# Kernel optimization log

Measured on AMD Instinct MI355X. Metric: run time of the kernel, lower is better.

The kernel has to match this reference:

```python
import jax, jax.numpy as jnp
import numpy as np

N = 100000      # nodes
E = 1600000     # edges (before self-loops)
IN = 128        # in_channels
H = 4           # heads
C = 32          # hidden_channels (per head)
HC = H * C      # 128, LayerNorm dim
NEG_SLOPE = 0.2
LN_EPS = 1e-5


def setup_inputs() -> dict:
    key = jax.random.key(0)
    ks = jax.random.split(key, 8)
    x = jax.random.normal(ks[0], (N, IN), dtype=jnp.float32)
    edge_index = jax.random.randint(ks[1], (2, E), 0, N, dtype=jnp.int64)
    edge_weight = jax.random.uniform(ks[2], (E,), dtype=jnp.float32)
    # GATConv parameters
    W = jax.random.normal(ks[3], (IN, HC), dtype=jnp.float32) * (1.0 / np.sqrt(IN))
    att_src = jax.random.normal(ks[4], (H, C), dtype=jnp.float32) * (1.0 / np.sqrt(C))
    att_dst = jax.random.normal(ks[5], (H, C), dtype=jnp.float32) * (1.0 / np.sqrt(C))
    bias = jnp.zeros((HC,), dtype=jnp.float32)
    # LayerNorm parameters
    gamma = jnp.ones((HC,), dtype=jnp.float32)
    beta = jnp.zeros((HC,), dtype=jnp.float32)
    return {"x": x, "edge_index": edge_index, "edge_weight": edge_weight,
            "W": W, "att_src": att_src, "att_dst": att_dst, "bias": bias,
            "gamma": gamma, "beta": beta}


def reference(x, edge_index, edge_weight, W, att_src, att_dst, bias, gamma, beta):
    # --- GATConv (heads=4, concat, add_self_loops=True) ---
    loops = jnp.arange(N, dtype=edge_index.dtype)
    ei = jnp.concatenate([edge_index, jnp.stack([loops, loops])], axis=1)  # [2, E+N]
    src, dst = ei[0], ei[1]

    xw = (x @ W).reshape(N, H, C)                       # [N, H, C]
    a_src = jnp.sum(xw * att_src, axis=-1)              # [N, H]
    a_dst = jnp.sum(xw * att_dst, axis=-1)              # [N, H]

    # per-edge attention logits, softmax grouped by destination node
    e = jax.nn.leaky_relu(a_src[src] + a_dst[dst], NEG_SLOPE)   # [E+N, H]
    m = jax.ops.segment_max(e, dst, num_segments=N)             # [N, H]
    ex = jnp.exp(e - m[dst])
    denom = jax.ops.segment_sum(ex, dst, num_segments=N)        # [N, H]
    alpha = ex / (denom[dst] + 1e-16)                           # [E+N, H]

    # weighted scatter-add of source features to destinations
    msg = alpha[:, :, None] * xw[src]                           # [E+N, H, C]
    out = jax.ops.segment_sum(msg, dst, num_segments=N)         # [N, H, C]
    out = out.reshape(N, HC) + bias                             # concat heads + bias

    # --- LayerNorm ---
    mu = jnp.mean(out, axis=-1, keepdims=True)
    var = jnp.var(out, axis=-1, keepdims=True)
    return gamma * (out - mu) / jnp.sqrt(var + LN_EPS) + beta
```

## Files before the change

### kernel.cpp

```cpp
#include <hip/hip_runtime.h>
#include <math.h>

#define NN 100000
#define EE 1600000
#define ETOT (EE + NN)
#define NBUK 512
#define NPB 196
#define CHUNK 3125
#define CAP 6144
#define GB 1563

typedef __attribute__((ext_vector_type(8))) short bf16x8;
typedef __attribute__((ext_vector_type(4))) float f32x4;

__device__ __forceinline__ unsigned short f2bf(float f) {
  unsigned int u = __float_as_uint(f);
  u = u + 0x7fffu + ((u >> 16) & 1u);
  return (unsigned short)(u >> 16);
}

__device__ __forceinline__ float lrelu_exp(float e) {
  e = (e > 0.f) ? e : 0.2f * e;
  return __expf(e);
}

__global__ __launch_bounds__(256) void k_gemm(const float* __restrict__ x,
                                              const float* __restrict__ W,
                                              const float* __restrict__ att_src,
                                              const float* __restrict__ att_dst,
                                              const int* __restrict__ ei,
                                              unsigned short* __restrict__ xwb,
                                              float* __restrict__ asrc,
                                              float* __restrict__ adst,
                                              int* __restrict__ H,
                                              int* __restrict__ Sc) {
  __shared__ __align__(16) unsigned short lds[17408];
  __shared__ float satt[256];
  __shared__ int hh[NBUK];
  int tid = threadIdx.x;

  if (blockIdx.x >= GB) {
    int j = blockIdx.x - GB;
    for (int i = tid; i < NBUK; i += 256) hh[i] = 0;
    __syncthreads();
    int e0 = j * CHUNK;
    for (int e = e0 + tid; e < e0 + CHUNK; e += 256) {
      int d = ei[(size_t)EE + e];
      atomicAdd(&hh[d / NPB], 1);
    }
    __syncthreads();
    for (int i = tid; i < NBUK; i += 256) H[j * NBUK + i] = hh[i];
    int* s = (int*)lds;
    int va = hh[tid], vb = hh[tid + 256];
    s[tid] = va;
    __syncthreads();
    for (int off = 1; off < 256; off <<= 1) {
      int tmp = (tid >= off) ? s[tid - off] : 0;
      __syncthreads();
      s[tid] += tmp;
      __syncthreads();
    }
    int Sa = s[tid], SaT = s[255];
    __syncthreads();
    s[tid] = vb;
    __syncthreads();
    for (int off = 1; off < 256; off <<= 1) {
      int tmp = (tid >= off) ? s[tid - off] : 0;
      __syncthreads();
      s[tid] += tmp;
      __syncthreads();
    }
    Sc[j * 512 + tid] = Sa - va;
    Sc[j * 512 + 256 + tid] = SaT + s[tid] - vb;
    return;
  }

  for (int i = tid; i < 16384; i += 256) {
    int k = i >> 7, n = i & 127;
    lds[n * 136 + k] = f2bf(W[i]);
  }
  if (tid < 128) satt[tid] = att_src[tid];
  else satt[tid] = att_dst[tid - 128];
  __syncthreads();

  int wv = tid >> 6, lane = tid & 63;
  int m = lane & 15, q = lane >> 4;
  int r = blockIdx.x * 64 + wv * 16 + m;
  bool rok = (r < NN);

  bf16x8 af[4];
#pragma unroll
  for (int kt = 0; kt < 4; kt++) {
    float4 v0 = make_float4(0.f, 0.f, 0.f, 0.f), v1 = v0;
    if (rok) {
      v0 = ((const float4*)x)[(size_t)r * 32 + kt * 8 + q * 2];
      v1 = ((const float4*)x)[(size_t)r * 32 + kt * 8 + q * 2 + 1];
    }
    af[kt][0] = (short)f2bf(v0.x); af[kt][1] = (short)f2bf(v0.y);
    af[kt][2] = (short)f2bf(v0.z); af[kt][3] = (short)f2bf(v0.w);
    af[kt][4] = (short)f2bf(v1.x); af[kt][5] = (short)f2bf(v1.y);
    af[kt][6] = (short)f2bf(v1.z); af[kt][7] = (short)f2bf(v1.w);
  }

  f32x4 acc[8];
#pragma unroll
  for (int nt = 0; nt < 8; nt++) acc[nt] = (f32x4){0.f, 0.f, 0.f, 0.f};

#pragma unroll
  for (int nt = 0; nt < 8; nt++) {
#pragma unroll
    for (int kt = 0; kt < 4; kt++) {
      bf16x8 bf = *((const bf16x8*)&lds[(nt * 16 + m) * 136 + kt * 32 + q * 8]);
      acc[nt] = __builtin_amdgcn_mfma_f32_16x16x32_bf16(af[kt], bf, acc[nt], 0, 0, 0);
    }
  }

  __syncthreads();
#pragma unroll
  for (int nt = 0; nt < 8; nt++)
#pragma unroll
    for (int rg = 0; rg < 4; rg++)
      lds[(wv * 16 + q * 4 + rg) * 128 + nt * 16 + m] = f2bf(acc[nt][rg]);
  __syncthreads();

  size_t base = (size_t)blockIdx.x * 16384;
  const size_t lim = (size_t)NN * 256;
  for (int i = tid; i < 1024; i += 256) {
    size_t off = base + (size_t)i * 16;
    if (off < lim) *((uint4*)((char*)xwb + off)) = ((const uint4*)lds)[i];
  }

  int row = tid >> 2, h = tid & 3;
  int node = blockIdx.x * 64 + row;
  if (node < NN) {
    float ss = 0.f, sd = 0.f;
#pragma unroll
    for (int cq = 0; cq < 4; cq++) {
      uint4 u = *((const uint4*)&lds[row * 128 + h * 32 + cq * 8]);
      int cb = h * 32 + cq * 8;
      float f0 = __uint_as_float(u.x << 16), f1 = __uint_as_float(u.x & 0xffff0000u);
      float f2 = __uint_as_float(u.y << 16), f3 = __uint_as_float(u.y & 0xffff0000u);
      float f4 = __uint_as_float(u.z << 16), f5 = __uint_as_float(u.z & 0xffff0000u);
      float f6 = __uint_as_float(u.w << 16), f7 = __uint_as_float(u.w & 0xffff0000u);
      ss += f0 * satt[cb] + f1 * satt[cb + 1] + f2 * satt[cb + 2] + f3 * satt[cb + 3] +
            f4 * satt[cb + 4] + f5 * satt[cb + 5] + f6 * satt[cb + 6] + f7 * satt[cb + 7];
      sd += f0 * satt[128 + cb] + f1 * satt[128 + cb + 1] + f2 * satt[128 + cb + 2] +
            f3 * satt[128 + cb + 3] + f4 * satt[128 + cb + 4] + f5 * satt[128 + cb + 5] +
            f6 * satt[128 + cb + 6] + f7 * satt[128 + cb + 7];
    }
    asrc[(size_t)node * 4 + h] = ss;
    adst[(size_t)node * 4 + h] = sd;
  }
}

__global__ __launch_bounds__(512) void k_s1(const int* __restrict__ H,
                                            int* __restrict__ R, int* __restrict__ T) {
  __shared__ int s[512];
  int b = blockIdx.x, t = threadIdx.x;
  int v = H[t * NBUK + b];
  s[t] = v;
  __syncthreads();
  for (int off = 1; off < 512; off <<= 1) {
    int tmp = (t >= off) ? s[t - off] : 0;
    __syncthreads();
    s[t] += tmp;
    __syncthreads();
  }
  R[b * 512 + t] = s[t] - v;
  if (t == 511) T[b] = s[511];
}

__global__ __launch_bounds__(512) void k_s2(const int* __restrict__ T,
                                            int* __restrict__ Base) {
  __shared__ int s2[512];
  int t = threadIdx.x;
  int v = T[t];
  int ncnt = NN - t * NPB;
  ncnt = (ncnt < 0) ? 0 : ((ncnt > NPB) ? NPB : ncnt);
  int w = v + ncnt;
  s2[t] = w;
  __syncthreads();
  for (int off = 1; off < 512; off <<= 1) {
    int tb = (t >= off) ? s2[t - off] : 0;
    __syncthreads();
    s2[t] += tb;
    __syncthreads();
  }
  Base[t] = s2[t] - w;
}

__global__ __launch_bounds__(256) void k_p3(const int* __restrict__ ei,
                                            const int* __restrict__ Sc,
                                            int* __restrict__ tmpb) {
  __shared__ int cur[NBUK];
  __shared__ int stage2[CHUNK];
  int j = blockIdx.x, t = threadIdx.x;
  for (int b = t; b < NBUK; b += 256) cur[b] = Sc[j * 512 + b];
  __syncthreads();
  int e0 = j * CHUNK;
  for (int e = e0 + t; e < e0 + CHUNK; e += 256) {
    int sv = ei[e];
    int dv = ei[(size_t)EE + e];
    int b = dv / NPB;
    int li = dv - b * NPB;
    int pos = atomicAdd(&cur[b], 1);
    stage2[pos] = (li << 17) | sv;
  }
  __syncthreads();
  for (int i = t; i < CHUNK; i += 256) tmpb[(size_t)j * CHUNK + i] = stage2[i];
}

__global__ __launch_bounds__(256) void k_p4(const int* __restrict__ tmpb,
                                            const int* __restrict__ H,
                                            const int* __restrict__ R,
                                            const int* __restrict__ T,
                                            const int* __restrict__ Sc,
                                            const int* __restrict__ Base,
                                            int* __restrict__ es, int* __restrict__ offs) {
  __shared__ int raw[CAP];
  __shared__ int stage[CAP];
  __shared__ int cnt[256];
  __shared__ int curn[NPB];
  int b = blockIdx.x, t = threadIdx.x;
  if (b == 0 && t == 0) offs[NN] = ETOT;
  int n0 = b * NPB;
  int nloc = NN - n0;
  if (nloc <= 0) return;
  if (nloc > NPB) nloc = NPB;
  int total = T[b];
  int bs = Base[b];
  cnt[t] = (t < nloc) ? 1 : 0;
  __syncthreads();
  for (int jj = t; jj < 512; jj += 256) {
    int st = Sc[jj * 512 + b];
    int ln = H[jj * NBUK + b];
    int rb = R[b * 512 + jj];
    const int* src = tmpb + (size_t)jj * CHUNK + st;
    for (int k = 0; k < ln; k++) {
      int w = src[k];
      int p = rb + k;
      if (p < CAP) raw[p] = w;
      atomicAdd(&cnt[w >> 17], 1);
    }
  }
  __syncthreads();
  int v = cnt[t];
  __syncthreads();
  for (int off = 1; off < 256; off <<= 1) {
    int tmp = (t >= off) ? cnt[t - off] : 0;
    __syncthreads();
    cnt[t] += tmp;
    __syncthreads();
  }
  int excl = cnt[t] - v;
  if (t < nloc) {
    offs[n0 + t] = bs + excl;
    curn[t] = excl + 1;
    if (excl < CAP) stage[excl] = n0 + t;
  }
  __syncthreads();
  int tl = (total < CAP) ? total : CAP;
  for (int e = t; e < tl; e += 256) {
    int u = raw[e];
    int pos = atomicAdd(&curn[u >> 17], 1);
    if (pos < CAP) stage[pos] = u & 0x1FFFF;
  }
  __syncthreads();
  int btot = total + nloc;
  if (btot > CAP) btot = CAP;
  for (int i = t; i < btot; i += 256) es[bs + i] = stage[i];
}

__global__ __launch_bounds__(256) void k_agg(const unsigned short* __restrict__ xwb,
                                             const float* __restrict__ asrc,
                                             const float* __restrict__ adst,
                                             const int* __restrict__ offs,
                                             const int* __restrict__ es,
                                             const float* __restrict__ bias,
                                             const float* __restrict__ gamma,
                                             const float* __restrict__ beta,
                                             float* __restrict__ out) {
  int lane = threadIdx.x & 63;
  int node = blockIdx.x * 4 + (threadIdx.x >> 6);
  int off0 = offs[node];
  int d = offs[node + 1] - off0;
  int h = lane >> 4;
  int he = lane & 3;
  int sel = lane >> 3;
  int c = lane * 2;

  float4 ad4 = *((const float4*)(adst + (size_t)node * 4));
  float ade = (he & 2) ? ((he & 1) ? ad4.w : ad4.z) : ((he & 1) ? ad4.y : ad4.x);

  const unsigned* xp = (const unsigned*)xwb + lane;
  const int* ep = es + off0;
  float ax0 = 0.f, ay0 = 0.f, ax1 = 0.f, ay1 = 0.f;
  float wsum = 0.f;

  int nb = (d + 7) >> 3;
  int4 sa = *((const int4*)(ep));
  int4 sb = *((const int4*)(ep + 4));

  for (int b = 0; b < nb; ++b) {
    int4 na = *((const int4*)(ep + (b + 1) * 8));
    int4 nbv = *((const int4*)(ep + (b + 1) * 8 + 4));

    int base = b * 8;
    int s0 = sa.x, s1 = sa.y, s2 = sa.z, s3 = sa.w;
    int s4 = sb.x, s5 = sb.y, s6 = sb.z, s7 = sb.w;
    bool full = (base + 8 <= d);
    if (!full) {
      s0 = (base + 0 < d) ? s0 : 0; s1 = (base + 1 < d) ? s1 : 0;
      s2 = (base + 2 < d) ? s2 : 0; s3 = (base + 3 < d) ? s3 : 0;
      s4 = (base + 4 < d) ? s4 : 0; s5 = (base + 5 < d) ? s5 : 0;
      s6 = (base + 6 < d) ? s6 : 0; s7 = (base + 7 < d) ? s7 : 0;
    }
    int t0 = (sel & 1) ? s1 : s0;
    int t1 = (sel & 1) ? s3 : s2;
    int t2 = (sel & 1) ? s5 : s4;
    int t3 = (sel & 1) ? s7 : s6;
    int p0 = (sel & 2) ? t1 : t0;
    int p1 = (sel & 2) ? t3 : t2;
    int se = (sel & 4) ? p1 : p0;
    float av = asrc[(size_t)(unsigned)se * 4u + (unsigned)he];

    unsigned u0 = xp[(unsigned)s0 * 64u];
    unsigned u1 = xp[(unsigned)s1 * 64u];
    unsigned u2 = xp[(unsigned)s2 * 64u];
    unsigned u3 = xp[(unsigned)s3 * 64u];
    unsigned u4 = xp[(unsigned)s4 * 64u];
    unsigned u5 = xp[(unsigned)s5 * 64u];
    unsigned u6 = xp[(unsigned)s6 * 64u];
    unsigned u7 = xp[(unsigned)s7 * 64u];

    float wl = lrelu_exp(av + ade);
    float w0 = __shfl(wl, 0 * 8 + h);
    float w1 = __shfl(wl, 1 * 8 + h);
    float w2 = __shfl(wl, 2 * 8 + h);
    float w3 = __shfl(wl, 3 * 8 + h);
    float w4 = __shfl(wl, 4 * 8 + h);
    float w5 = __shfl(wl, 5 * 8 + h);
    float w6 = __shfl(wl, 6 * 8 + h);
    float w7 = __shfl(wl, 7 * 8 + h);
    if (!full) {
      w0 = (base + 0 < d) ? w0 : 0.f; w1 = (base + 1 < d) ? w1 : 0.f;
      w2 = (base + 2 < d) ? w2 : 0.f; w3 = (base + 3 < d) ? w3 : 0.f;
      w4 = (base + 4 < d) ? w4 : 0.f; w5 = (base + 5 < d) ? w5 : 0.f;
      w6 = (base + 6 < d) ? w6 : 0.f; w7 = (base + 7 < d) ? w7 : 0.f;
    }
    wsum += ((w0 + w1) + (w2 + w3)) + ((w4 + w5) + (w6 + w7));
    ax0 = fmaf(w0, __uint_as_float(u0 << 16), ax0);
    ay0 = fmaf(w0, __uint_as_float(u0 & 0xffff0000u), ay0);
    ax1 = fmaf(w1, __uint_as_float(u1 << 16), ax1);
    ay1 = fmaf(w1, __uint_as_float(u1 & 0xffff0000u), ay1);
    ax0 = fmaf(w2, __uint_as_float(u2 << 16), ax0);
    ay0 = fmaf(w2, __uint_as_float(u2 & 0xffff0000u), ay0);
    ax1 = fmaf(w3, __uint_as_float(u3 << 16), ax1);
    ay1 = fmaf(w3, __uint_as_float(u3 & 0xffff0000u), ay1);
    ax0 = fmaf(w4, __uint_as_float(u4 << 16), ax0);
    ay0 = fmaf(w4, __uint_as_float(u4 & 0xffff0000u), ay0);
    ax1 = fmaf(w5, __uint_as_float(u5 << 16), ax1);
    ay1 = fmaf(w5, __uint_as_float(u5 & 0xffff0000u), ay1);
    ax0 = fmaf(w6, __uint_as_float(u6 << 16), ax0);
    ay0 = fmaf(w6, __uint_as_float(u6 & 0xffff0000u), ay0);
    ax1 = fmaf(w7, __uint_as_float(u7 << 16), ax1);
    ay1 = fmaf(w7, __uint_as_float(u7 & 0xffff0000u), ay1);

    sa = na; sb = nbv;
  }

  float accx = ax0 + ax1, accy = ay0 + ay1;
  float rn = 1.f / (wsum + 1e-16f);

  float vx = accx * rn + bias[c];
  float vy = accy * rn + bias[c + 1];
  float sum = vx + vy, sq = vx * vx + vy * vy;
#pragma unroll
  for (int o = 32; o; o >>= 1) {
    sum += __shfl_xor(sum, o);
    sq += __shfl_xor(sq, o);
  }
  float mean = sum * (1.f / 128.f);
  float var = sq * (1.f / 128.f) - mean * mean;
  float rs = rsqrtf(var + 1e-5f);
  float o0 = gamma[c] * (vx - mean) * rs + beta[c];
  float o1 = gamma[c + 1] * (vy - mean) * rs + beta[c + 1];
  float2 ov; ov.x = o0; ov.y = o1;
  *((float2*)(out + (size_t)node * 128 + c)) = ov;
}

extern "C" void kernel_launch(void* const* d_in, const int* in_sizes, int n_in,
                              void* d_out, int out_size, void* d_ws, size_t ws_size,
                              hipStream_t stream) {
  const float* x = (const float*)d_in[0];
  const int* ei = (const int*)d_in[1];
  const float* W = (const float*)d_in[3];
  const float* att_src = (const float*)d_in[4];
  const float* att_dst = (const float*)d_in[5];
  const float* bias = (const float*)d_in[6];
  const float* gamma = (const float*)d_in[7];
  const float* beta = (const float*)d_in[8];
  float* out = (float*)d_out;

  char* p = (char*)d_ws;
  auto alloc = [&](size_t bytes) -> char* {
    char* r = p;
    p += (bytes + 255) & ~(size_t)255;
    return r;
  };
  unsigned short* xwb = (unsigned short*)alloc((size_t)NN * 128 * 2);
  float* asrc = (float*)alloc((size_t)NN * 4 * 4);
  float* adst = (float*)alloc((size_t)NN * 4 * 4);
  int* es = (int*)alloc((size_t)ETOT * 4 + 128);
  int* offs = (int*)alloc((size_t)(NN + 1) * 4);
  int* tmpb = (int*)alloc((size_t)EE * 4);
  int* H = (int*)alloc((size_t)512 * NBUK * 4);
  int* Sc = (int*)alloc((size_t)512 * NBUK * 4);
  int* R = (int*)alloc((size_t)NBUK * 512 * 4);
  int* T = (int*)alloc((size_t)NBUK * 4);
  int* Base = (int*)alloc((size_t)(NBUK + 1) * 4);

  k_gemm<<<GB + NBUK, 256, 0, stream>>>(x, W, att_src, att_dst, ei, xwb, asrc, adst, H, Sc);
  k_s1<<<NBUK, 512, 0, stream>>>(H, R, T);
  k_s2<<<1, 512, 0, stream>>>(T, Base);
  k_p3<<<512, 256, 0, stream>>>(ei, Sc, tmpb);
  k_p4<<<NBUK, 256, 0, stream>>>(tmpb, H, R, T, Sc, Base, es, offs);
  k_agg<<<NN / 4, 256, 0, stream>>>(xwb, asrc, adst, offs, es, bias, gamma, beta, out);
}
```

Measured before the change: 249.2 us.

## Merge scan and partition kernels and compute bucket bases inside p4

The per-bucket column scan (k_s1) and the edge partition pass (k_p3) now run as two block ranges of a single launch, since neither depends on the other. The single-block scan of bucket totals (k_s2) is removed; instead each k_p4 block reduces the T entries of the buckets before it to get its base offset. This cuts two kernel launches and their serialization gaps from the CSR build. In exchange, every k_p4 block does a redundant reduction over up to 512 totals, and the scan kernel now runs with 256 threads covering 512 entries in two passes.

```diff
diff --git a/kernel.cpp b/kernel.cpp
--- a/kernel.cpp
+++ b/kernel.cpp
@@ -24,16 +24,16 @@
   return __expf(e);
 }
 
-__global__ __launch_bounds__(256) void k_gemm(const float* __restrict__ x,
-                                              const float* __restrict__ W,
-                                              const float* __restrict__ att_src,
-                                              const float* __restrict__ att_dst,
-                                              const int* __restrict__ ei,
-                                              unsigned short* __restrict__ xwb,
-                                              float* __restrict__ asrc,
-                                              float* __restrict__ adst,
-                                              int* __restrict__ H,
-                                              int* __restrict__ Sc) {
+__global__ __launch_bounds__(256) void k_front(const float* __restrict__ x,
+                                               const float* __restrict__ W,
+                                               const float* __restrict__ att_src,
+                                               const float* __restrict__ att_dst,
+                                               const int* __restrict__ ei,
+                                               unsigned short* __restrict__ xwb,
+                                               float* __restrict__ asrc,
+                                               float* __restrict__ adst,
+                                               int* __restrict__ H,
+                                               int* __restrict__ Sc) {
   __shared__ __align__(16) unsigned short lds[17408];
   __shared__ float satt[256];
   __shared__ int hh[NBUK];
@@ -153,57 +153,55 @@
   }
 }
 
-__global__ __launch_bounds__(512) void k_s1(const int* __restrict__ H,
-                                            int* __restrict__ R, int* __restrict__ T) {
-  __shared__ int s[512];
-  int b = blockIdx.x, t = threadIdx.x;
-  int v = H[t * NBUK + b];
-  s[t] = v;
-  __syncthreads();
-  for (int off = 1; off < 512; off <<= 1) {
-    int tmp = (t >= off) ? s[t - off] : 0;
-    __syncthreads();
-    s[t] += tmp;
-    __syncthreads();
-  }
-  R[b * 512 + t] = s[t] - v;
-  if (t == 511) T[b] = s[511];
-}
-
-__global__ __launch_bounds__(512) void k_s2(const int* __restrict__ T,
-                                            int* __restrict__ Base) {
-  __shared__ int s2[512];
+__global__ __launch_bounds__(256) void k_s1p3(const int* __restrict__ ei,
+                                              const int* __restrict__ H,
+                                              const int* __restrict__ Sc,
+                                              int* __restrict__ R, int* __restrict__ T,
+                                              int* __restrict__ tmpb) {
+  __shared__ int sh[512 + CHUNK];
   int t = threadIdx.x;
-  int v = T[t];
-  int ncnt = NN - t * NPB;
-  ncnt = (ncnt < 0) ? 0 : ((ncnt > NPB) ? NPB : ncnt);
-  int w = v + ncnt;
-  s2[t] = w;
-  __syncthreads();
-  for (int off = 1; off < 512; off <<= 1) {
-    int tb = (t >= off) ? s2[t - off] : 0;
-    __syncthreads();
-    s2[t] += tb;
-    __syncthreads();
-  }
-  Base[t] = s2[t] - w;
-}
-
-__global__ __launch_bounds__(256) void k_p3(const int* __restrict__ ei,
-                                            const int* __restrict__ Sc,
-                                            int* __restrict__ tmpb) {
-  __shared__ int cur[NBUK];
-  __shared__ int stage2[CHUNK];
-  int j = blockIdx.x, t = threadIdx.x;
-  for (int b = t; b < NBUK; b += 256) cur[b] = Sc[j * 512 + b];
+
+  if (blockIdx.x < NBUK) {
+    int b = blockIdx.x;
+    int* s = sh;
+    int va = H[t * NBUK + b];
+    int vb = H[(t + 256) * NBUK + b];
+    s[t] = va;
+    __syncthreads();
+    for (int off = 1; off < 256; off <<= 1) {
+      int tmp = (t >= off) ? s[t - off] : 0;
+      __syncthreads();
+      s[t] += tmp;
+      __syncthreads();
+    }
+    int Sa = s[t], SaT = s[255];
+    __syncthreads();
+    s[t] = vb;
+    __syncthreads();
+    for (int off = 1; off < 256; off <<= 1) {
+      int tmp = (t >= off) ? s[t - off] : 0;
+      __syncthreads();
+      s[t] += tmp;
+      __syncthreads();
+    }
+    R[b * 512 + t] = Sa - va;
+    R[b * 512 + 256 + t] = SaT + s[t] - vb;
+    if (t == 255) T[b] = SaT + s[255];
+    return;
+  }
+
+  int j = blockIdx.x - NBUK;
+  int* cur = sh;
+  int* stage2 = sh + 512;
+  for (int b2 = t; b2 < NBUK; b2 += 256) cur[b2] = Sc[j * 512 + b2];
   __syncthreads();
   int e0 = j * CHUNK;
   for (int e = e0 + t; e < e0 + CHUNK; e += 256) {
     int sv = ei[e];
     int dv = ei[(size_t)EE + e];
-    int b = dv / NPB;
-    int li = dv - b * NPB;
-    int pos = atomicAdd(&cur[b], 1);
+    int b2 = dv / NPB;
+    int li = dv - b2 * NPB;
+    int pos = atomicAdd(&cur[b2], 1);
     stage2[pos] = (li << 17) | sv;
   }
   __syncthreads();
@@ -215,7 +213,6 @@
                                             const int* __restrict__ R,
                                             const int* __restrict__ T,
                                             const int* __restrict__ Sc,
-                                            const int* __restrict__ Base,
                                             int* __restrict__ es, int* __restrict__ offs) {
   __shared__ int raw[CAP];
   __shared__ int stage[CAP];
@@ -228,7 +225,16 @@
   if (nloc <= 0) return;
   if (nloc > NPB) nloc = NPB;
   int total = T[b];
-  int bs = Base[b];
+  int pacc = 0;
+  for (int i = t; i < b; i += 256) pacc += T[i];
+  cnt[t] = pacc;
+  __syncthreads();
+  for (int off = 128; off; off >>= 1) {
+    if (t < off) cnt[t] += cnt[t + off];
+    __syncthreads();
+  }
+  int bs = cnt[0] + n0;
+  __syncthreads();
   cnt[t] = (t < nloc) ? 1 : 0;
   __syncthreads();
   for (int jj = t; jj < 512; jj += 256) {
@@ -418,12 +424,9 @@
   int* Sc = (int*)alloc((size_t)512 * NBUK * 4);
   int* R = (int*)alloc((size_t)NBUK * 512 * 4);
   int* T = (int*)alloc((size_t)NBUK * 4);
-  int* Base = (int*)alloc((size_t)(NBUK + 1) * 4);
-
-  k_gemm<<<GB + NBUK, 256, 0, stream>>>(x, W, att_src, att_dst, ei, xwb, asrc, adst, H, Sc);
-  k_s1<<<NBUK, 512, 0, stream>>>(H, R, T);
-  k_s2<<<1, 512, 0, stream>>>(T, Base);
-  k_p3<<<512, 256, 0, stream>>>(ei, Sc, tmpb);
-  k_p4<<<NBUK, 256, 0, stream>>>(tmpb, H, R, T, Sc, Base, es, offs);
+
+  k_front<<<GB + NBUK, 256, 0, stream>>>(x, W, att_src, att_dst, ei, xwb, asrc, adst, H, Sc);
+  k_s1p3<<<2 * NBUK, 256, 0, stream>>>(ei, H, Sc, R, T, tmpb);
+  k_p4<<<NBUK, 256, 0, stream>>>(tmpb, H, R, T, Sc, es, offs);
   k_agg<<<NN / 4, 256, 0, stream>>>(xwb, asrc, adst, offs, es, bias, gamma, beta, out);
 }
```

Result: faster. 243.9 us (-2.2%).
